# Performance work log

Hardware: AMD Instinct MI355X
Metric: run time of the kernel (lower is better)

Reference implementation:

```python
import jax, jax.numpy as jnp
import numpy as np

HEADS = 8
DIM_HEAD = 64
SCALE = DIM_HEAD ** -0.5
K = 7


def _conv(x, w, stride):
    return jax.lax.conv_general_dilated(
        x, w, window_strides=(stride, stride), padding='VALID',
        dimension_numbers=('NHWC', 'HWIO', 'NHWC'))


def _split_heads(t):
    # 'b x y (h d) -> (b h) (x y) d'
    b, X, Y, hd = t.shape
    d = hd // HEADS
    t = t.reshape(b, X, Y, HEADS, d)
    t = t.transpose(0, 3, 1, 2, 4)  # b h x y d
    return t.reshape(b * HEADS, X * Y, d)


def setup_inputs() -> dict:
    key = jax.random.key(0)
    ks = jax.random.split(key, 6)
    dim, inner = 256, HEADS * DIM_HEAD
    x = jax.random.normal(ks[0], (8, 84, 84, dim), dtype=jnp.float32)
    w_q = jax.random.normal(ks[1], (1, 1, dim, inner), dtype=jnp.float32) * 0.02
    w_kv = jax.random.normal(ks[2], (K, K, dim, 2 * inner), dtype=jnp.float32) * 0.02
    w_out = jax.random.normal(ks[3], (1, 1, inner, dim), dtype=jnp.float32) * 0.02
    b_out = jnp.zeros((dim,), dtype=jnp.float32)
    return {"x": x, "w_q": w_q, "w_kv": w_kv, "w_out": w_out, "b_out": b_out}


def reference(x, w_q, w_kv, w_out, b_out):
    b, X, Y, _ = x.shape
    q = _conv(x, w_q, 1)          # [b, X, Y, inner]
    kv = _conv(x, w_kv, K)        # [b, X/k, Y/k, 2*inner]
    k, v = jnp.split(kv, 2, axis=-1)
    q = _split_heads(q)           # [(b h), XY, d]
    k = _split_heads(k)           # [(b h), xy, d]
    v = _split_heads(v)
    dots = jnp.einsum('bid,bjd->bij', q, k) * SCALE
    attn = jax.nn.softmax(dots, axis=-1)
    out = jnp.einsum('bij,bjd->bid', attn, v)  # [(b h), XY, d]
    out = out.reshape(b, HEADS, X, Y, DIM_HEAD).transpose(0, 2, 3, 1, 4)
    out = out.reshape(b, X, Y, HEADS * DIM_HEAD)
    out = _conv(out, w_out, 1) + b_out  # dropout rate 0 -> identity
    return out
```

## Files before the change

### kernel.cpp

```cpp
#include <hip/hip_runtime.h>

typedef unsigned short u16;
typedef __bf16 bf16x8 __attribute__((ext_vector_type(8)));
typedef __bf16 bf16x4 __attribute__((ext_vector_type(4)));
typedef float f32x4 __attribute__((ext_vector_type(4)));

__device__ __forceinline__ u16 f2b(float f) {
    __bf16 h = (__bf16)f;
    return __builtin_bit_cast(u16, h);
}
__device__ __forceinline__ unsigned pk2(float a, float b) {
    return (unsigned)f2b(a) | ((unsigned)f2b(b) << 16);
}

__device__ __forceinline__ int xcd_chunk(int wg, int n) {
    int q = n >> 3, r = n & 7;
    int x = wg & 7, i = wg >> 3;
    return (x < r ? x * (q + 1) : r * (q + 1) + (x - r) * q) + i;
}

#define GLOAD_LDS16(src, dst)                                              \
    __builtin_amdgcn_global_load_lds(                                      \
        (const __attribute__((address_space(1))) void*)(src),              \
        (__attribute__((address_space(3))) void*)(dst), 16, 0, 0)

__global__ __launch_bounds__(256) void k_pack_x(const float* __restrict__ x,
                                                u16* __restrict__ xp) {
    int v = blockIdx.x * 256 + threadIdx.x;
    int c0 = (v & 31) << 3;
    int pix = v >> 5;
    int b = pix / 7056;
    int r = pix - b * 7056;
    int y = r / 84;
    int xx = r - y * 84;
    int opix = (b * 144 + (y / 7) * 12 + (xx / 7)) * 49 + (y % 7) * 7 + (xx % 7);
    const float4* src = reinterpret_cast<const float4*>(x + ((size_t)pix << 8) + c0);
    float4 f0 = src[0], f1 = src[1];
    bf16x8 o = {(__bf16)f0.x, (__bf16)f0.y, (__bf16)f0.z, (__bf16)f0.w,
                (__bf16)f1.x, (__bf16)f1.y, (__bf16)f1.z, (__bf16)f1.w};
    *reinterpret_cast<bf16x8*>(xp + ((size_t)opix << 8) + c0) = o;
}

__global__ __launch_bounds__(256) void k_tconv(const float* __restrict__ in,
                                               u16* __restrict__ out, int R, int C,
                                               float scale, int permk) {
    __shared__ float tile[32][33];
    int c0 = blockIdx.x << 5, r0 = blockIdx.y << 5;
    int tx = threadIdx.x, ty = threadIdx.y;
#pragma unroll
    for (int i = 0; i < 4; i++)
        tile[ty + (i << 3)][tx] = in[(size_t)(r0 + ty + (i << 3)) * C + c0 + tx];
    __syncthreads();
    int k = r0 + tx;
    int kw = permk ? ((k & ~63) | ((k & 15) << 2) | ((k >> 4) & 3)) : k;
#pragma unroll
    for (int i = 0; i < 4; i++)
        out[(size_t)(c0 + ty + (i << 3)) * R + kw] = f2b(tile[tx][ty + (i << 3)] * scale);
}

__global__ __launch_bounds__(256) void k_kvproj(const u16* __restrict__ xp,
                                                const u16* __restrict__ wkvT,
                                                float* __restrict__ parts) {
    __shared__ u16 As[8192];
    __shared__ u16 Bs[8192];
    const int lin = xcd_chunk(blockIdx.x, 504);
    const int mt = lin % 9;
    const int ntsp = lin / 9;
    const int nt = ntsp & 7;
    const int sp = ntsp >> 3;
    const int tid = threadIdx.x;
    const int wave = tid >> 6, lane = tid & 63;
    const int wr = wave >> 1, wc = wave & 1;
    const int lrow = lane & 15, lkg = lane >> 4;
    const u16* Ag = xp + (size_t)(mt * 128) * 12544 + sp * 1792;
    const u16* Bg = wkvT + (size_t)(nt * 128) * 12544 + sp * 1792;
    const int srow = lane >> 3, scol = (lane & 7) << 3;
    f32x4 acc[4][4];
#pragma unroll
    for (int m = 0; m < 4; m++)
#pragma unroll
        for (int n = 0; n < 4; n++)
#pragma unroll
            for (int i = 0; i < 4; i++) acc[m][n][i] = 0.f;

    for (int ks = 0; ks < 28; ks++) {
        const int k0 = ks << 6;
        __syncthreads();
#pragma unroll
        for (int j = 0; j < 4; j++) {
            const int c = (wave << 2) + j;
            const int row = (c << 3) + srow;
            GLOAD_LDS16(Ag + (size_t)row * 12544 + k0 + scol, As + (c << 9));
            GLOAD_LDS16(Bg + (size_t)row * 12544 + k0 + scol, Bs + (c << 9));
        }
        __syncthreads();
#pragma unroll
        for (int kk = 0; kk < 2; kk++) {
            const int ko = (kk << 5) + (lkg << 3);
            bf16x8 a[4], bb[4];
#pragma unroll
            for (int m = 0; m < 4; m++)
                a[m] = *reinterpret_cast<const bf16x8*>(As + (((wr << 6) + (m << 4) + lrow) << 6) + ko);
#pragma unroll
            for (int n = 0; n < 4; n++)
                bb[n] = *reinterpret_cast<const bf16x8*>(Bs + (((wc << 6) + (n << 4) + lrow) << 6) + ko);
#pragma unroll
            for (int m = 0; m < 4; m++)
#pragma unroll
                for (int n = 0; n < 4; n++)
                    acc[m][n] = __builtin_amdgcn_mfma_f32_16x16x32_bf16(a[m], bb[n], acc[m][n], 0, 0, 0);
        }
    }
    float* outp = parts + (size_t)sp * 1179648;
#pragma unroll
    for (int m = 0; m < 4; m++)
#pragma unroll
        for (int n = 0; n < 4; n++)
#pragma unroll
            for (int i = 0; i < 4; i++) {
                int row = (mt << 7) + (wr << 6) + (m << 4) + (lkg << 2) + i;
                int col = (nt << 7) + (wc << 6) + (n << 4) + lrow;
                outp[(size_t)row * 1024 + col] = acc[m][n][i];
            }
}

__global__ __launch_bounds__(256) void k_kvfin(const float* __restrict__ parts,
                                               u16* __restrict__ Kf, u16* __restrict__ Vf) {
    int idx = blockIdx.x * 256 + threadIdx.x;
    int m = idx >> 10, n = idx & 1023;
    float s = 0.f;
#pragma unroll
    for (int sp = 0; sp < 7; sp++) s += parts[(size_t)sp * 1179648 + idx];
    int b = m / 144, pi = m - b * 144;
    int h = (n & 511) >> 6, d = n & 63;
    int bh = (b << 3) + h;
    if (n < 512) {
        int fc = pi >> 4, lr = pi & 15;
        int ks = d >> 5, lg = (d >> 3) & 3, e = d & 7;
        Kf[((((size_t)bh * 9 + fc) << 1) + ks) * 512 + (((lg << 4) + lr) << 3) + e] = f2b(s);
    } else {
        int nf = d >> 4, lr = d & 15;
        int ks = pi >> 5;
        int e = (((pi >> 4) & 1) << 2) | (pi & 3);
        int lg = (pi >> 2) & 3;
        Vf[(((size_t)bh * 4 + nf) * 5 + ks) * 512 + (((lg << 4) + lr) << 3) + e] = f2b(s);
    }
}

__global__ __launch_bounds__(256) void k_qproj(const u16* __restrict__ xp,
                                               const u16* __restrict__ wqT,
                                               u16* __restrict__ Qf) {
    __shared__ u16 As[128][72];
    __shared__ u16 Bs[128][72];
    const int lin = xcd_chunk(blockIdx.x, 1764);
    const int nt = lin & 3, mt = lin >> 2;
    const int tid = threadIdx.x;
    const int wave = tid >> 6, lane = tid & 63;
    const int wr = wave >> 1, wc = wave & 1;
    const int lrow = lane & 15, lkg = lane >> 4;
    const u16* Ag = xp + (size_t)(mt * 128) * 256;
    const u16* Bg = wqT + (size_t)(nt * 128) * 256;
    const int srow = tid >> 3, scol = (tid & 7) << 3;
    f32x4 acc[4][4];
#pragma unroll
    for (int m = 0; m < 4; m++)
#pragma unroll
        for (int n = 0; n < 4; n++)
#pragma unroll
            for (int i = 0; i < 4; i++) acc[m][n][i] = 0.f;

    for (int ks = 0; ks < 4; ks++) {
        const int k0 = ks * 64;
        __syncthreads();
#pragma unroll
        for (int p = 0; p < 4; p++) {
            int rr = srow + (p << 5);
            *reinterpret_cast<bf16x8*>(&As[rr][scol]) =
                *reinterpret_cast<const bf16x8*>(Ag + (size_t)rr * 256 + k0 + scol);
            *reinterpret_cast<bf16x8*>(&Bs[rr][scol]) =
                *reinterpret_cast<const bf16x8*>(Bg + (size_t)rr * 256 + k0 + scol);
        }
        __syncthreads();
#pragma unroll
        for (int kk = 0; kk < 2; kk++) {
            const int ko = (kk << 5) + (lkg << 3);
            bf16x8 a[4], bb[4];
#pragma unroll
            for (int m = 0; m < 4; m++)
                a[m] = *reinterpret_cast<const bf16x8*>(&As[(wr << 6) + (m << 4) + lrow][ko]);
#pragma unroll
            for (int n = 0; n < 4; n++)
                bb[n] = *reinterpret_cast<const bf16x8*>(&Bs[(wc << 6) + (n << 4) + lrow][ko]);
#pragma unroll
            for (int m = 0; m < 4; m++)
#pragma unroll
                for (int n = 0; n < 4; n++)
                    acc[m][n] = __builtin_amdgcn_mfma_f32_16x16x32_bf16(a[m], bb[n], acc[m][n], 0, 0, 0);
        }
    }
#pragma unroll
    for (int m = 0; m < 4; m++)
#pragma unroll
        for (int n = 0; n < 4; n++)
#pragma unroll
            for (int i = 0; i < 4; i++) {
                int row = (mt << 7) + (wr << 6) + (m << 4) + (lkg << 2) + i;
                int col = (nt << 7) + (wc << 6) + (n << 4) + lrow;
                int b = row / 7056, pp = row - b * 7056;
                int h = col >> 6, d = col & 63;
                int bh = (b << 3) + h;
                int tt = pp >> 4, flr = pp & 15;
                int fks = d >> 5, flg = (d >> 3) & 3, fe = d & 7;
                Qf[((((size_t)bh * 441 + tt) << 1) + fks) * 512 + (((flg << 4) + flr) << 3) + fe] =
                    f2b(acc[m][n][i]);
            }
}

__global__ __launch_bounds__(128, 4) void k_attn(const u16* __restrict__ Qf,
                                                 const u16* __restrict__ Kf,
                                                 const u16* __restrict__ Vf,
                                                 u16* __restrict__ O) {
    const int wv = threadIdx.x >> 6, lane = threadIdx.x & 63;
    const int t = blockIdx.x;
    const int h = (blockIdx.y << 1) + wv;
    const int b = blockIdx.z;
    const int lrow = lane & 15, lkg = lane >> 4;
    const int bh = (b << 3) + h;
    const int l8 = lane << 3;

    const u16* Qg = Qf + ((((size_t)bh * 441 + t) << 1) << 9);
    const u16* Kg = Kf + (((size_t)bh * 9) << 10);
    const u16* Vg = Vf + ((size_t)bh * 20) * 512;

    f32x4 da[9];
#pragma unroll
    for (int fc = 0; fc < 9; fc++)
#pragma unroll
        for (int i = 0; i < 4; i++) da[fc][i] = 0.f;
#pragma unroll
    for (int ks = 0; ks < 2; ks++) {
        bf16x8 aq = *reinterpret_cast<const bf16x8*>(Qg + (ks << 9) + l8);
#pragma unroll
        for (int fc = 0; fc < 9; fc++) {
            bf16x8 bk = *reinterpret_cast<const bf16x8*>(Kg + ((((fc << 1) + ks)) << 9) + l8);
            da[fc] = __builtin_amdgcn_mfma_f32_16x16x32_bf16(bk, aq, da[fc], 0, 0, 0);
        }
    }

    float mx = -1e30f;
#pragma unroll
    for (int fc = 0; fc < 9; fc++)
#pragma unroll
        for (int i = 0; i < 4; i++) mx = fmaxf(mx, da[fc][i]);
    mx = fmaxf(mx, __shfl_xor(mx, 16));
    mx = fmaxf(mx, __shfl_xor(mx, 32));
    float sum = 0.f;
#pragma unroll
    for (int fc = 0; fc < 9; fc++)
#pragma unroll
        for (int i = 0; i < 4; i++) {
            float v = __expf(da[fc][i] - mx);
            da[fc][i] = v;
            sum += v;
        }
    sum += __shfl_xor(sum, 16);
    sum += __shfl_xor(sum, 32);
    float inv = 1.0f / sum;
    unsigned pw[9][2];
#pragma unroll
    for (int fc = 0; fc < 9; fc++) {
        pw[fc][0] = pk2(da[fc][0] * inv, da[fc][1] * inv);
        pw[fc][1] = pk2(da[fc][2] * inv, da[fc][3] * inv);
    }

    f32x4 oa[4];
#pragma unroll
    for (int n = 0; n < 4; n++)
#pragma unroll
        for (int i = 0; i < 4; i++) oa[n][i] = 0.f;
#pragma unroll
    for (int ks = 0; ks < 5; ks++) {
        uint4 pav;
        if (ks < 4)
            pav = uint4{pw[2 * ks][0], pw[2 * ks][1], pw[2 * ks + 1][0], pw[2 * ks + 1][1]};
        else
            pav = uint4{pw[8][0], pw[8][1], 0u, 0u};
        bf16x8 pa = __builtin_bit_cast(bf16x8, pav);
#pragma unroll
        for (int n = 0; n < 4; n++) {
            bf16x8 bv = *reinterpret_cast<const bf16x8*>(Vg + ((size_t)(n * 5 + ks) << 9) + l8);
            oa[n] = __builtin_amdgcn_mfma_f32_16x16x32_bf16(pa, bv, oa[n], 0, 0, 0);
        }
    }

#pragma unroll
    for (int i = 0; i < 4; i++) {
        int r = (lkg << 2) + i;
        int q = (t << 4) + r;
        int pi = q / 49, pos = q - pi * 49;
        int y = (pi / 12) * 7 + pos / 7;
        int xx = (pi - (pi / 12) * 12) * 7 + (pos - (pos / 7) * 7);
        bf16x4 ov = {(__bf16)oa[0][i], (__bf16)oa[1][i], (__bf16)oa[2][i], (__bf16)oa[3][i]};
        *reinterpret_cast<bf16x4*>(O + (((size_t)b * 7056 + y * 84 + xx) << 9) +
                                   (h << 6) + (lrow << 2)) = ov;
    }
}

__global__ __launch_bounds__(256) void k_outproj(const u16* __restrict__ A,
                                                 const u16* __restrict__ BT,
                                                 const float* __restrict__ bias,
                                                 float* __restrict__ out) {
    __shared__ u16 As[128][72];
    __shared__ u16 Bs[128][72];
    const int lin = xcd_chunk(blockIdx.x, 882);
    const int nt = lin & 1, mt = lin >> 1;
    const int tid = threadIdx.x;
    const int wave = tid >> 6, lane = tid & 63;
    const int wr = wave >> 1, wc = wave & 1;
    const int lrow = lane & 15, lkg = lane >> 4;
    const u16* Ag = A + (size_t)(mt * 128) * 512;
    const u16* Bg = BT + (size_t)(nt * 128) * 512;
    const int srow = tid >> 3, scol = (tid & 7) << 3;
    f32x4 acc[4][4];
#pragma unroll
    for (int m = 0; m < 4; m++)
#pragma unroll
        for (int n = 0; n < 4; n++)
#pragma unroll
            for (int i = 0; i < 4; i++) acc[m][n][i] = 0.f;

    for (int ks = 0; ks < 8; ks++) {
        const int k0 = ks * 64;
        __syncthreads();
#pragma unroll
        for (int p = 0; p < 4; p++) {
            int rr = srow + (p << 5);
            *reinterpret_cast<bf16x8*>(&As[rr][scol]) =
                *reinterpret_cast<const bf16x8*>(Ag + (size_t)rr * 512 + k0 + scol);
            *reinterpret_cast<bf16x8*>(&Bs[rr][scol]) =
                *reinterpret_cast<const bf16x8*>(Bg + (size_t)rr * 512 + k0 + scol);
        }
        __syncthreads();
#pragma unroll
        for (int kk = 0; kk < 2; kk++) {
            const int ko = (kk << 5) + (lkg << 3);
            bf16x8 a[4], bb[4];
#pragma unroll
            for (int m = 0; m < 4; m++)
                a[m] = *reinterpret_cast<const bf16x8*>(&As[(wr << 6) + (m << 4) + lrow][ko]);
#pragma unroll
            for (int n = 0; n < 4; n++)
                bb[n] = *reinterpret_cast<const bf16x8*>(&Bs[(wc << 6) + (n << 4) + lrow][ko]);
#pragma unroll
            for (int m = 0; m < 4; m++)
#pragma unroll
                for (int n = 0; n < 4; n++)
                    acc[m][n] = __builtin_amdgcn_mfma_f32_16x16x32_bf16(a[m], bb[n], acc[m][n], 0, 0, 0);
        }
    }
#pragma unroll
    for (int m = 0; m < 4; m++)
#pragma unroll
        for (int n = 0; n < 4; n++)
#pragma unroll
            for (int i = 0; i < 4; i++) {
                int row = (mt << 7) + (wr << 6) + (m << 4) + (lkg << 2) + i;
                int col = (nt << 7) + (wc << 6) + (n << 4) + lrow;
                out[(size_t)row * 256 + col] = acc[m][n][i] + bias[col];
            }
}

extern "C" void kernel_launch(void* const* d_in, const int* in_sizes, int n_in,
                              void* d_out, int out_size, void* d_ws, size_t ws_size,
                              hipStream_t stream) {
    const float* x = (const float*)d_in[0];
    const float* w_q = (const float*)d_in[1];
    const float* w_kv = (const float*)d_in[2];
    const float* w_out = (const float*)d_in[3];
    const float* b_out = (const float*)d_in[4];
    float* out = (float*)d_out;

    char* ws = (char*)d_ws;
    size_t off = 0;
    auto alloc = [&](size_t bytes) -> char* {
        char* p = ws + off;
        off = (off + bytes + 255) & ~(size_t)255;
        return p;
    };
    u16* xp = (u16*)alloc(28901376ull);
    u16* wqT = (u16*)alloc(262144ull);
    u16* woutT = (u16*)alloc(262144ull);
    u16* Kf = (u16*)alloc(1179648ull);
    u16* Vf = (u16*)alloc(1310720ull);
    u16* O = (u16*)alloc(57802752ull);
    u16* wkvT = (u16*)alloc(25690112ull);
    float* parts = (float*)alloc(33030144ull);
    u16* Qf = (u16*)wkvT;

    hipMemsetAsync(Vf, 0, 1310720ull, stream);
    k_pack_x<<<7056, 256, 0, stream>>>(x, xp);
    k_tconv<<<dim3(32, 392), dim3(32, 8), 0, stream>>>(w_kv, wkvT, 12544, 1024, 1.0f, 0);
    k_tconv<<<dim3(16, 8), dim3(32, 8), 0, stream>>>(w_q, wqT, 256, 512, 0.125f, 0);
    k_tconv<<<dim3(8, 16), dim3(32, 8), 0, stream>>>(w_out, woutT, 512, 256, 1.0f, 1);
    k_kvproj<<<504, 256, 0, stream>>>(xp, wkvT, parts);
    k_kvfin<<<4608, 256, 0, stream>>>(parts, Kf, Vf);
    k_qproj<<<1764, 256, 0, stream>>>(xp, wqT, Qf);
    k_attn<<<dim3(441, 4, 8), 128, 0, stream>>>(Qf, Kf, Vf, O);
    k_outproj<<<882, 256, 0, stream>>>(O, woutT, b_out, out);
}
```

Baseline: 222.4 us.

## Halve kvproj N-tile, swizzle LDS layout, vectorize kvfin partial-sum reads

The K/V projection GEMM now uses 128x64 tiles instead of 128x128. This doubles the grid from 504 to 1008 workgroups so the CUs are better filled, and lowers register and LDS use per block. The LDS columns are XOR-swizzled by row in both the global-to-LDS load and the MFMA fragment reads to avoid bank conflicts. The split-K reduction kernel now reads float4 partials and handles four outputs per thread, cutting load instructions. Smaller tiles reread the A operand more often across N tiles.

Result: no change. 223.3 us (+0.4%).

```diff
diff --git a/kernel.cpp b/kernel.cpp
--- a/kernel.cpp
+++ b/kernel.cpp
@@ -62,24 +62,25 @@
                                                 const u16* __restrict__ wkvT,
                                                 float* __restrict__ parts) {
     __shared__ u16 As[8192];
-    __shared__ u16 Bs[8192];
-    const int lin = xcd_chunk(blockIdx.x, 504);
+    __shared__ u16 Bs[4096];
+    const int lin = xcd_chunk(blockIdx.x, 1008);
     const int mt = lin % 9;
-    const int ntsp = lin / 9;
-    const int nt = ntsp & 7;
-    const int sp = ntsp >> 3;
+    const int rest = lin / 9;
+    const int nt = rest & 15;
+    const int sp = rest >> 4;
     const int tid = threadIdx.x;
     const int wave = tid >> 6, lane = tid & 63;
     const int wr = wave >> 1, wc = wave & 1;
     const int lrow = lane & 15, lkg = lane >> 4;
     const u16* Ag = xp + (size_t)(mt * 128) * 12544 + sp * 1792;
-    const u16* Bg = wkvT + (size_t)(nt * 128) * 12544 + sp * 1792;
-    const int srow = lane >> 3, scol = (lane & 7) << 3;
-    f32x4 acc[4][4];
-#pragma unroll
-    for (int m = 0; m < 4; m++)
-#pragma unroll
-        for (int n = 0; n < 4; n++)
+    const u16* Bg = wkvT + (size_t)(nt * 64) * 12544 + sp * 1792;
+    const int srow = lane >> 3;
+    const int scol_sw = (((lane & 7) ^ srow) << 3);
+    f32x4 acc[4][2];
+#pragma unroll
+    for (int m = 0; m < 4; m++)
+#pragma unroll
+        for (int n = 0; n < 2; n++)
 #pragma unroll
             for (int i = 0; i < 4; i++) acc[m][n][i] = 0.f;
 
@@ -90,24 +91,30 @@
         for (int j = 0; j < 4; j++) {
             const int c = (wave << 2) + j;
             const int row = (c << 3) + srow;
-            GLOAD_LDS16(Ag + (size_t)row * 12544 + k0 + scol, As + (c << 9));
-            GLOAD_LDS16(Bg + (size_t)row * 12544 + k0 + scol, Bs + (c << 9));
+            GLOAD_LDS16(Ag + (size_t)row * 12544 + k0 + scol_sw, As + (c << 9));
+        }
+#pragma unroll
+        for (int j = 0; j < 2; j++) {
+            const int c = (wave << 1) + j;
+            const int row = (c << 3) + srow;
+            GLOAD_LDS16(Bg + (size_t)row * 12544 + k0 + scol_sw, Bs + (c << 9));
         }
         __syncthreads();
 #pragma unroll
         for (int kk = 0; kk < 2; kk++) {
-            const int ko = (kk << 5) + (lkg << 3);
-            bf16x8 a[4], bb[4];
-#pragma unroll
-            for (int m = 0; m < 4; m++)
-                a[m] = *reinterpret_cast<const bf16x8*>(As + (((wr << 6) + (m << 4) + lrow) << 6) + ko);
-#pragma unroll
-            for (int n = 0; n < 4; n++)
-                bb[n] = *reinterpret_cast<const bf16x8*>(Bs + (((wc << 6) + (n << 4) + lrow) << 6) + ko);
-#pragma unroll
-            for (int m = 0; m < 4; m++)
-#pragma unroll
-                for (int n = 0; n < 4; n++)
+            const int sig = (kk << 2) + lkg;
+            const int sw = ((sig ^ (lrow & 7)) << 3);
+            bf16x8 a[4], bb[2];
+#pragma unroll
+            for (int m = 0; m < 4; m++)
+                a[m] = *reinterpret_cast<const bf16x8*>(As + (((wr << 6) + (m << 4) + lrow) << 6) + sw);
+#pragma unroll
+            for (int n = 0; n < 2; n++)
+                bb[n] = *reinterpret_cast<const bf16x8*>(Bs + (((wc << 5) + (n << 4) + lrow) << 6) + sw);
+#pragma unroll
+            for (int m = 0; m < 4; m++)
+#pragma unroll
+                for (int n = 0; n < 2; n++)
                     acc[m][n] = __builtin_amdgcn_mfma_f32_16x16x32_bf16(a[m], bb[n], acc[m][n], 0, 0, 0);
         }
     }
@@ -115,35 +122,45 @@
 #pragma unroll
     for (int m = 0; m < 4; m++)
 #pragma unroll
-        for (int n = 0; n < 4; n++)
+        for (int n = 0; n < 2; n++)
 #pragma unroll
             for (int i = 0; i < 4; i++) {
                 int row = (mt << 7) + (wr << 6) + (m << 4) + (lkg << 2) + i;
-                int col = (nt << 7) + (wc << 6) + (n << 4) + lrow;
+                int col = (nt << 6) + (wc << 5) + (n << 4) + lrow;
                 outp[(size_t)row * 1024 + col] = acc[m][n][i];
             }
 }
 
 __global__ __launch_bounds__(256) void k_kvfin(const float* __restrict__ parts,
                                                u16* __restrict__ Kf, u16* __restrict__ Vf) {
-    int idx = blockIdx.x * 256 + threadIdx.x;
-    int m = idx >> 10, n = idx & 1023;
-    float s = 0.f;
-#pragma unroll
-    for (int sp = 0; sp < 7; sp++) s += parts[(size_t)sp * 1179648 + idx];
+    int v = blockIdx.x * 256 + threadIdx.x;
+    int m = v >> 8;
+    int n0 = (v & 255) << 2;
+    float4 s = {0.f, 0.f, 0.f, 0.f};
+#pragma unroll
+    for (int sp = 0; sp < 7; sp++) {
+        float4 p = *reinterpret_cast<const float4*>(parts + (size_t)sp * 1179648 +
+                                                    (size_t)m * 1024 + n0);
+        s.x += p.x; s.y += p.y; s.z += p.z; s.w += p.w;
+    }
     int b = m / 144, pi = m - b * 144;
-    int h = (n & 511) >> 6, d = n & 63;
-    int bh = (b << 3) + h;
-    if (n < 512) {
-        int fc = pi >> 4, lr = pi & 15;
-        int ks = d >> 5, lg = (d >> 3) & 3, e = d & 7;
-        Kf[((((size_t)bh * 9 + fc) << 1) + ks) * 512 + (((lg << 4) + lr) << 3) + e] = f2b(s);
-    } else {
-        int nf = d >> 4, lr = d & 15;
-        int ks = pi >> 5;
-        int e = (((pi >> 4) & 1) << 2) | (pi & 3);
-        int lg = (pi >> 2) & 3;
-        Vf[(((size_t)bh * 4 + nf) * 5 + ks) * 512 + (((lg << 4) + lr) << 3) + e] = f2b(s);
+    float sv[4] = {s.x, s.y, s.z, s.w};
+#pragma unroll
+    for (int e4 = 0; e4 < 4; e4++) {
+        int n = n0 + e4;
+        int h = (n & 511) >> 6, d = n & 63;
+        int bh = (b << 3) + h;
+        if (n < 512) {
+            int fc = pi >> 4, lr = pi & 15;
+            int ks = d >> 5, lg = (d >> 3) & 3, e = d & 7;
+            Kf[((((size_t)bh * 9 + fc) << 1) + ks) * 512 + (((lg << 4) + lr) << 3) + e] = f2b(sv[e4]);
+        } else {
+            int nf = d >> 4, lr = d & 15;
+            int ks = pi >> 5;
+            int e = (((pi >> 4) & 1) << 2) | (pi & 3);
+            int lg = (pi >> 2) & 3;
+            Vf[(((size_t)bh * 4 + nf) * 5 + ks) * 512 + (((lg << 4) + lr) << 3) + e] = f2b(sv[e4]);
+        }
     }
 }
 
@@ -402,8 +419,8 @@
     k_tconv<<<dim3(32, 392), dim3(32, 8), 0, stream>>>(w_kv, wkvT, 12544, 1024, 1.0f, 0);
     k_tconv<<<dim3(16, 8), dim3(32, 8), 0, stream>>>(w_q, wqT, 256, 512, 0.125f, 0);
     k_tconv<<<dim3(8, 16), dim3(32, 8), 0, stream>>>(w_out, woutT, 512, 256, 1.0f, 1);
-    k_kvproj<<<504, 256, 0, stream>>>(xp, wkvT, parts);
-    k_kvfin<<<4608, 256, 0, stream>>>(parts, Kf, Vf);
+    k_kvproj<<<1008, 256, 0, stream>>>(xp, wkvT, parts);
+    k_kvfin<<<1152, 256, 0, stream>>>(parts, Kf, Vf);
     k_qproj<<<1764, 256, 0, stream>>>(xp, wqT, Qf);
     k_attn<<<dim3(441, 4, 8), 128, 0, stream>>>(Qf, Kf, Vf, O);
     k_outproj<<<882, 256, 0, stream>>>(O, woutT, b_out, out);
```
